# Performance work log

Measured on AMD Instinct MI355X. Metric: run time of the kernel, lower is better.

## Reference

```python
import jax, jax.numpy as jnp
import numpy as np

B, E, S = 64, 256, 32        # batch, projection_size (=MHA embed dim), seq_l
H = 16                        # MHA heads
D_FINAL = 10                  # label space
K_CLASSES = D_FINAL * (D_FINAL - 1) // 2 + 1  # 46, header output dim
N_PATIENTS = 8
P_PAIRS = N_PATIENTS * (B // N_PATIENTS) ** 2  # 512 same-patient pairs (static)


def _pair_lookup(D):
    # class id of sorted label pair: (0,0)->0, then (a,b) a<b in lexicographic
    # order, matching torch.unique(rows of triu meshgrid) ordering.
    lut = np.zeros((D, D), np.int32)
    idx = 1
    for a in range(D):
        for b in range(a + 1, D):
            lut[a, b] = idx
            lut[b, a] = idx
            idx += 1
    return lut


def setup_inputs():
    ks = jax.random.split(jax.random.key(0), 10)
    s = 1.0 / np.sqrt(E)
    return {
        "features": jax.random.normal(ks[0], (B, E, S), jnp.float32),
        "labels0": jax.random.randint(ks[1], (B,), 0, D_FINAL, jnp.int32),
        "labels1": (jnp.arange(B, dtype=jnp.int32) // (B // N_PATIENTS)),
        "in_proj_w": jax.random.normal(ks[2], (3 * E, E), jnp.float32) * s,
        "in_proj_b": jax.random.normal(ks[3], (3 * E,), jnp.float32) * 0.01,
        "out_proj_w": jax.random.normal(ks[4], (E, E), jnp.float32) * s,
        "out_proj_b": jax.random.normal(ks[5], (E,), jnp.float32) * 0.01,
        "final_w": jax.random.normal(ks[6], (1, S), jnp.float32) * (1.0 / np.sqrt(S)),
        "final_b": jax.random.normal(ks[7], (1,), jnp.float32) * 0.01,
        "header_w": jax.random.normal(ks[8], (K_CLASSES, E), jnp.float32) * s,
        "header_b": jax.random.normal(ks[9], (K_CLASSES,), jnp.float32) * 0.01,
    }


def reference(features, labels0, labels1, in_proj_w, in_proj_b, out_proj_w,
              out_proj_b, final_w, final_b, header_w, header_b):
    # ---- pair selection: (i, j) with same patient id (labels1) ----
    mask = (labels1[:, None] == labels1[None, :]).reshape(-1)  # (B*B,)
    sel = jnp.nonzero(mask, size=P_PAIRS, fill_value=0)[0]      # row-major order
    valid = (jnp.arange(P_PAIRS) < mask.sum()).astype(jnp.float32)
    i_idx, j_idx = sel // B, sel % B                            # (P,), (P,)

    # ---- pair class labels: sorted (l_i, l_j), equal labels -> (0, 0) ----
    a, b = labels0[i_idx], labels0[j_idx]
    eq = a == b
    lo = jnp.where(eq, 0, jnp.minimum(a, b))
    hi = jnp.where(eq, 0, jnp.maximum(a, b))
    lut = jnp.asarray(_pair_lookup(D_FINAL))
    y = lut[lo, hi]                                             # (P,) class ids

    # ---- gather pair features; torch permutes to (2, P, seq_l, C) ----
    q_in = jnp.transpose(features[i_idx], (0, 2, 1))  # (P, S, E) query
    kv_in = jnp.transpose(features[j_idx], (0, 2, 1))  # (P, S, E) key/value

    # ---- MultiheadAttention (eval, dropout off); L = pair axis P, N = S ----
    Wq, Wk, Wv = jnp.split(in_proj_w, 3, axis=0)
    bq, bk, bv = jnp.split(in_proj_b, 3, axis=0)
    hd = E // H
    q = (q_in @ Wq.T + bq).reshape(P_PAIRS, S, H, hd)
    k = (kv_in @ Wk.T + bk).reshape(P_PAIRS, S, H, hd)
    v = (kv_in @ Wv.T + bv).reshape(P_PAIRS, S, H, hd)
    scores = jnp.einsum('lshd,mshd->shlm', q, k) / np.sqrt(hd)  # (S,H,P,P)
    attn = jax.nn.softmax(scores, axis=-1)
    o = jnp.einsum('shlm,mshd->lshd', attn, v).reshape(P_PAIRS, S, E)
    o = o @ out_proj_w.T + out_proj_b                           # (P, S, E)

    # ---- backbone.final: Linear over the seq axis (S -> 1), squeeze ----
    h = jnp.einsum('pse,s->pe', o, final_w[0]) + final_b[0]     # (P, E)
    logits = h @ header_w.T + header_b                          # (P, K)

    # ---- inverse-frequency class weights over selected pairs ----
    counts = jnp.zeros(K_CLASSES, jnp.float32).at[y].add(valid)
    w = jnp.where(counts > 0, 1.0 / jnp.maximum(counts, 1.0), 0.0)

    # ---- weighted cross-entropy (torch semantics: / sum of weights) ----
    nll = -jax.nn.log_softmax(logits, axis=-1)[jnp.arange(P_PAIRS), y]
    wy = w[y] * valid
    loss = jnp.sum(wy * nll) / jnp.sum(wy)
    return loss
```

## Files before the change

### kernel.cpp

```cpp
#include <hip/hip_runtime.h>
#include <math.h>

#define B_ 64
#define E_ 256
#define S_ 32
#define H_ 16
#define P_ 512
#define KC_ 46

#define WS_CM     0
#define WS_WK     256
#define WS_INVDEN 3328
#define WS_C      3392
#define WS_M      3584
#define WS_WB     16384
#define WS_XF     114688
#define WS_OPART  1949696

typedef short bf16x8 __attribute__((ext_vector_type(8)));
typedef float f32x4  __attribute__((ext_vector_type(4)));

__device__ __forceinline__ ushort f2bf(float f) {
  unsigned u = __float_as_uint(f);
  u = (u + 0x7FFFu + ((u >> 16) & 1u)) >> 16;
  return (ushort)u;
}

__global__ __launch_bounds__(256) void k_prep(
    const float* __restrict__ feat, const float* __restrict__ w,
    const int* __restrict__ labels0, const int* __restrict__ labels1,
    const float* __restrict__ wout, const float* __restrict__ bout,
    const float* __restrict__ fw, const float* __restrict__ fbi,
    const float* __restrict__ hw, const float* __restrict__ hb,
    float* __restrict__ ws, float* __restrict__ out) {
  __shared__ float sm[8448];
  const int bid = blockIdx.x, t = threadIdx.x;
  if (bid < 24) {
    const float4* src = (const float4*)w;
    ushort* dstW = (ushort*)(ws + WS_WB);
#pragma unroll
    for (int i = 0; i < 8; ++i) {
      int idx = bid*2048 + i*256 + t;
      float4 v = src[idx];
      ushort4 o;
      o.x = f2bf(v.x); o.y = f2bf(v.y); o.z = f2bf(v.z); o.w = f2bf(v.w);
      *(ushort4*)(dstW + (size_t)idx*4) = o;
    }
  } else if (bid < 88) {
    const int b = bid - 24;
    const float4* fb = (const float4*)(feat + (size_t)b*(E_*S_));
#pragma unroll
    for (int i = 0; i < 8; ++i) {
      int idx = i*256 + t; int e = idx >> 3, s4 = (idx & 7)*4;
      float4 v = fb[idx];
      sm[e*33 + s4+0] = v.x; sm[e*33 + s4+1] = v.y;
      sm[e*33 + s4+2] = v.z; sm[e*33 + s4+3] = v.w;
    }
    __syncthreads();
    const int s = t >> 3, eb = (t & 7) * 32;
    ushort* dstX = (ushort*)(ws + WS_XF) + (size_t)s*(B_*E_) + (size_t)b*E_ + eb;
#pragma unroll
    for (int g = 0; g < 4; ++g) {
      ushort tmp[8];
#pragma unroll
      for (int u = 0; u < 8; ++u) tmp[u] = f2bf(sm[(eb + g*8 + u)*33 + s]);
      *(uint4*)(dstX + g*8) = *(uint4*)tmp;
    }
  } else if (bid == 88) {
    float* csh = sm;
    float* cls = sm + 64;
    float* wsh = sm + 112;
    float* den = sm + 160;
    float* Wk  = sm + 192;
    int* scan = (int*)(sm + 3200);
    int* l0   = (int*)(sm + 3456);
    int* l1   = (int*)(sm + 3520);
    int* seli = (int*)(sm + 3584);
    int* selj = (int*)(sm + 4096);
    if (t < 64) { l0[t] = labels0[t]; l1[t] = labels1[t]; csh[t] = 0.f; }
    if (t < KC_) cls[t] = 0.f;
    if (t == 0) den[0] = 0.f;
    for (int i = t; i < 2944; i += 256) Wk[i] = 0.f;
    __syncthreads();
    unsigned bits = 0; int c = 0;
    for (int u = 0; u < 16; ++u) {
      int idx = t*16 + u;
      if (l1[idx>>6] == l1[idx&63]) { bits |= 1u<<u; ++c; }
    }
    scan[t] = c; __syncthreads();
    for (int off = 1; off < 256; off <<= 1) {
      int v = (t >= off) ? scan[t-off] : 0;
      __syncthreads();
      scan[t] += v;
      __syncthreads();
    }
    const int total = scan[255];
    int rank = scan[t] - c;
    for (int p = t; p < P_; p += 256)
      if (p >= total) { seli[p] = 0; selj[p] = 0; }
    for (int u = 0; u < 16; ++u) {
      if (bits & (1u<<u)) {
        if (rank < P_) { int idx = t*16+u; seli[rank] = idx>>6; selj[rank] = idx&63; }
        ++rank;
      }
    }
    __syncthreads();
    int ii[2], yy[2]; float vv[2];
#pragma unroll
    for (int r = 0; r < 2; ++r) {
      int p = t + r*256;
      int i = seli[p], j = selj[p];
      atomicAdd(&csh[j], 1.0f);
      int la = l0[i], lb = l0[j];
      int y;
      if (la == lb) y = 0;
      else {
        int lo = la < lb ? la : lb, hi = la < lb ? lb : la;
        y = 1 + lo*9 - (lo*(lo-1))/2 + (hi-lo-1);
      }
      float v = (p < total) ? 1.f : 0.f;
      if (v > 0.f) atomicAdd(&cls[y], 1.f);
      ii[r] = i; yy[r] = y; vv[r] = v;
    }
    __syncthreads();
    if (t < KC_) {
      float cv = cls[t];
      wsh[t] = cv > 0.f ? 1.0f/cv : 0.f;
      if (cv > 0.f) atomicAdd(den, 1.0f);
    }
    __syncthreads();
#pragma unroll
    for (int r = 0; r < 2; ++r)
      if (vv[r] > 0.f) atomicAdd(&Wk[ii[r]*KC_ + yy[r]], wsh[yy[r]]);
    __syncthreads();
    if (t < 64) ws[WS_CM + t] = csh[t];
    for (int i = t; i < 2944; i += 256) ws[WS_WK + i] = Wk[i];
    if (t == 0) ws[WS_INVDEN] = 1.0f / den[0];
  } else if (bid < 135) {
    int k = bid - 89;
    float* hwsh = sm;
    float* redA = sm + 256;
    float* redB = sm + 512;
    hwsh[t] = hw[k*E_ + t];
    __syncthreads();
    float a0 = 0.f;
#pragma unroll 8
    for (int e = 0; e < E_; ++e) a0 = fmaf(hwsh[e], wout[e*E_ + t], a0);
    ws[WS_M + k*E_ + t] = a0;
    redA[t] = hwsh[t];
    redB[t] = hwsh[t]*bout[t];
    __syncthreads();
    for (int off = 128; off > 0; off >>= 1) {
      if (t < off) { redA[t] += redA[t+off]; redB[t] += redB[t+off]; }
      __syncthreads();
    }
    if (t == 0) {
      float sfw = 0.f;
      for (int s = 0; s < S_; ++s) sfw += fw[s];
      ws[WS_C + k] = fbi[0]*redA[0] + sfw*redB[0] + hb[k];
    }
  } else {
    if (t == 0) out[0] = 0.f;
  }
}

__global__ __launch_bounds__(256) void k_attn(
    const float* __restrict__ bias, const float* __restrict__ fw,
    float* __restrict__ ws) {
  __shared__ float qT[16*68], kT[16*68], vs[64*20], sc[64*68], cm[64];
  const int s = blockIdx.x >> 4, h = blockIdx.x & 15;
  const int t = threadIdx.x;
  const int w = t >> 6, L = t & 63, lane16 = L & 15, quad = L >> 4;
  const int a = t >> 2, dq = t & 3;
  {
    const short* WB = (const short*)(ws + WS_WB);
    const short* XF = (const short*)(ws + WS_XF);
    const short* brow  = XF + (size_t)s*(B_*E_) + (size_t)(w*16 + lane16)*E_ + quad*8;
    const short* arowQ = WB + (size_t)(      h*16 + lane16)*E_ + quad*8;
    const short* arowK = WB + (size_t)(256 + h*16 + lane16)*E_ + quad*8;
    const short* arowV = WB + (size_t)(512 + h*16 + lane16)*E_ + quad*8;
    f32x4 accQ = {0.f,0.f,0.f,0.f}, accK = {0.f,0.f,0.f,0.f}, accV = {0.f,0.f,0.f,0.f};
#pragma unroll
    for (int k = 0; k < 8; ++k) {
      bf16x8 bv = *(const bf16x8*)(brow  + k*32);
      bf16x8 aq = *(const bf16x8*)(arowQ + k*32);
      bf16x8 ak = *(const bf16x8*)(arowK + k*32);
      bf16x8 av = *(const bf16x8*)(arowV + k*32);
      accQ = __builtin_amdgcn_mfma_f32_16x16x32_bf16(aq, bv, accQ, 0, 0, 0);
      accK = __builtin_amdgcn_mfma_f32_16x16x32_bf16(ak, bv, accK, 0, 0, 0);
      accV = __builtin_amdgcn_mfma_f32_16x16x32_bf16(av, bv, accV, 0, 0, 0);
    }
    float4 bq = *(const float4*)(bias +        h*16 + quad*4);
    float4 bk = *(const float4*)(bias + 256 + h*16 + quad*4);
    float4 bv2 = *(const float4*)(bias + 512 + h*16 + quad*4);
    const float bqa[4] = {bq.x,bq.y,bq.z,bq.w};
    const float bka[4] = {bk.x,bk.y,bk.z,bk.w};
    const float bva[4] = {bv2.x,bv2.y,bv2.z,bv2.w};
    const int ag = w*16 + lane16;
#pragma unroll
    for (int r = 0; r < 4; ++r) {
      int d = quad*4 + r;
      qT[d*68 + ag] = (accQ[r] + bqa[r]) * 0.25f;
      kT[d*68 + ag] =  accK[r] + bka[r];
      vs[ag*20 + d] =  accV[r] + bva[r];
    }
  }
  if (t < 64) cm[t] = ws[WS_CM + t];
  __syncthreads();
  {
    const int ta = t & 15, tb = t >> 4;
    float sa[4][4];
#pragma unroll
    for (int r = 0; r < 4; ++r)
#pragma unroll
      for (int c = 0; c < 4; ++c) sa[r][c] = 0.f;
#pragma unroll
    for (int d = 0; d < 16; ++d) {
      float4 qv = *(float4*)(qT + d*68 + ta*4);
      float4 kv = *(float4*)(kT + d*68 + tb*4);
      float qr[4] = {qv.x,qv.y,qv.z,qv.w};
      float kc[4] = {kv.x,kv.y,kv.z,kv.w};
#pragma unroll
      for (int r = 0; r < 4; ++r)
#pragma unroll
        for (int c = 0; c < 4; ++c) sa[r][c] = fmaf(qr[r], kc[c], sa[r][c]);
    }
#pragma unroll
    for (int r = 0; r < 4; ++r)
      *(float4*)(sc + (ta*4+r)*68 + tb*4) =
          make_float4(sa[r][0], sa[r][1], sa[r][2], sa[r][3]);
  }
  __syncthreads();
  {
    float pv[16], cmv[16];
#pragma unroll
    for (int i4 = 0; i4 < 4; ++i4) {
      float4 v = *(float4*)(sc + a*68 + dq*16 + i4*4);
      pv[i4*4+0] = v.x; pv[i4*4+1] = v.y; pv[i4*4+2] = v.z; pv[i4*4+3] = v.w;
    }
#pragma unroll
    for (int i = 0; i < 16; ++i) cmv[i] = cm[dq*16 + i];
    float Mx = -1e30f;
#pragma unroll
    for (int i = 0; i < 16; ++i) if (cmv[i] > 0.f) Mx = fmaxf(Mx, pv[i]);
    Mx = fmaxf(Mx, __shfl_xor(Mx, 1));
    Mx = fmaxf(Mx, __shfl_xor(Mx, 2));
    float z = 0.f;
#pragma unroll
    for (int i = 0; i < 16; ++i) {
      float e = (cmv[i] > 0.f) ? cmv[i]*__expf(pv[i]-Mx) : 0.f;
      pv[i] = e; z += e;
    }
    z += __shfl_xor(z, 1);
    z += __shfl_xor(z, 2);
    float rz = 1.0f / z;
#pragma unroll
    for (int i4 = 0; i4 < 4; ++i4)
      *(float4*)(sc + a*68 + dq*16 + i4*4) =
          make_float4(pv[i4*4+0]*rz, pv[i4*4+1]*rz,
                      pv[i4*4+2]*rz, pv[i4*4+3]*rz);
  }
  __syncthreads();
  {
    const int g = t >> 6, l = t & 63;
    const int ar = g*16 + (l >> 2), d4 = (l & 3)*4;
    float o0 = 0.f, o1 = 0.f, o2 = 0.f, o3 = 0.f;
#pragma unroll 4
    for (int b4 = 0; b4 < 64; b4 += 4) {
      float4 p4 = *(float4*)(sc + ar*68 + b4);
      float4 va = *(float4*)(vs + (b4+0)*20 + d4);
      float4 vb = *(float4*)(vs + (b4+1)*20 + d4);
      float4 vc = *(float4*)(vs + (b4+2)*20 + d4);
      float4 vd = *(float4*)(vs + (b4+3)*20 + d4);
      o0 = fmaf(p4.x, va.x, fmaf(p4.y, vb.x, fmaf(p4.z, vc.x, fmaf(p4.w, vd.x, o0))));
      o1 = fmaf(p4.x, va.y, fmaf(p4.y, vb.y, fmaf(p4.z, vc.y, fmaf(p4.w, vd.y, o1))));
      o2 = fmaf(p4.x, va.z, fmaf(p4.y, vb.z, fmaf(p4.z, vc.z, fmaf(p4.w, vd.z, o2))));
      o3 = fmaf(p4.x, va.w, fmaf(p4.y, vb.w, fmaf(p4.z, vc.w, fmaf(p4.w, vd.w, o3))));
    }
    const float fwS = fw[s];
    float* dst = ws + WS_OPART + (size_t)s*(H_*B_*16) + h*(B_*16) + t*4;
    *(float4*)dst = make_float4(fwS*o0, fwS*o1, fwS*o2, fwS*o3);
  }
}

__global__ __launch_bounds__(256) void k_final(
    const float* __restrict__ ws, float* __restrict__ out) {
  const int aa = blockIdx.x, t = threadIdx.x;
  __shared__ float oh[256], lg[64];
  {
    const float* op = ws + WS_OPART + (t>>4)*(B_*16) + aa*16 + (t&15);
    float acc = 0.f;
#pragma unroll
    for (int s = 0; s < S_; ++s) acc += op[(size_t)s*(H_*B_*16)];
    oh[t] = acc;
  }
  __syncthreads();
  const int k = t >> 2, q = t & 3;
  if (k < KC_) {
    float lv = 0.f;
    const float4* M4 = (const float4*)(ws + WS_M + k*E_ + q*64);
    const float4* o4 = (const float4*)(oh + q*64);
#pragma unroll
    for (int j = 0; j < 16; ++j) {
      float4 m = M4[j], o = o4[j];
      lv = fmaf(m.x, o.x, lv); lv = fmaf(m.y, o.y, lv);
      lv = fmaf(m.z, o.z, lv); lv = fmaf(m.w, o.w, lv);
    }
    lv += __shfl_xor(lv, 1);
    lv += __shfl_xor(lv, 2);
    if (q == 0) lg[k] = lv + ws[WS_C + k];
  }
  __syncthreads();
  if (t < 64) {
    float x = (t < KC_) ? lg[t] : -1e30f;
    float Mx = x;
#pragma unroll
    for (int off = 1; off < 64; off <<= 1) Mx = fmaxf(Mx, __shfl_xor(Mx, off));
    float z = (t < KC_) ? __expf(x - Mx) : 0.f;
#pragma unroll
    for (int off = 1; off < 64; off <<= 1) z += __shfl_xor(z, off);
    float lse = Mx + __logf(z);
    float term = (t < KC_) ? ws[WS_WK + aa*KC_ + t] * (lse - x) : 0.f;
#pragma unroll
    for (int off = 1; off < 64; off <<= 1) term += __shfl_xor(term, off);
    if (t == 0) atomicAdd(out, term * ws[WS_INVDEN]);
  }
}

extern "C" void kernel_launch(void* const* d_in, const int* in_sizes, int n_in,
                              void* d_out, int out_size, void* d_ws, size_t ws_size,
                              hipStream_t stream) {
  const float* feat    = (const float*)d_in[0];
  const int*   labels0 = (const int*)d_in[1];
  const int*   labels1 = (const int*)d_in[2];
  const float* ipw     = (const float*)d_in[3];
  const float* ipb     = (const float*)d_in[4];
  const float* opw     = (const float*)d_in[5];
  const float* opb     = (const float*)d_in[6];
  const float* fw      = (const float*)d_in[7];
  const float* fbi     = (const float*)d_in[8];
  const float* hw      = (const float*)d_in[9];
  const float* hb      = (const float*)d_in[10];
  float* out = (float*)d_out;
  float* ws  = (float*)d_ws;

  k_prep<<<136, 256, 0, stream>>>(feat, ipw, labels0, labels1, opw, opb, fw,
                                  fbi, hw, hb, ws, out);
  k_attn<<<512, 256, 0, stream>>>(ipb, fw, ws);
  k_final<<<64, 256, 0, stream>>>(ws, out);
}
```

Measured before the change: 105.4 us.

## Move pair-selection and output-projection work from prep into attention and final kernels

```diff
diff --git a/kernel.cpp b/kernel.cpp
--- a/kernel.cpp
+++ b/kernel.cpp
@@ -8,11 +8,6 @@
 #define P_ 512
 #define KC_ 46
 
-#define WS_CM     0
-#define WS_WK     256
-#define WS_INVDEN 3328
-#define WS_C      3392
-#define WS_M      3584
 #define WS_WB     16384
 #define WS_XF     114688
 #define WS_OPART  1949696
@@ -26,12 +21,14 @@
   return (ushort)u;
 }
 
+__device__ __forceinline__ int pairclass(int la, int lb) {
+  if (la == lb) return 0;
+  int lo = la < lb ? la : lb, hi = la < lb ? lb : la;
+  return 1 + lo*9 - (lo*(lo-1))/2 + (hi - lo - 1);
+}
+
 __global__ __launch_bounds__(256) void k_prep(
     const float* __restrict__ feat, const float* __restrict__ w,
-    const int* __restrict__ labels0, const int* __restrict__ labels1,
-    const float* __restrict__ wout, const float* __restrict__ bout,
-    const float* __restrict__ fw, const float* __restrict__ fbi,
-    const float* __restrict__ hw, const float* __restrict__ hb,
     float* __restrict__ ws, float* __restrict__ out) {
   __shared__ float sm[8448];
   const int bid = blockIdx.x, t = threadIdx.x;
@@ -66,99 +63,6 @@
       for (int u = 0; u < 8; ++u) tmp[u] = f2bf(sm[(eb + g*8 + u)*33 + s]);
       *(uint4*)(dstX + g*8) = *(uint4*)tmp;
     }
-  } else if (bid == 88) {
-    float* csh = sm;
-    float* cls = sm + 64;
-    float* wsh = sm + 112;
-    float* den = sm + 160;
-    float* Wk  = sm + 192;
-    int* scan = (int*)(sm + 3200);
-    int* l0   = (int*)(sm + 3456);
-    int* l1   = (int*)(sm + 3520);
-    int* seli = (int*)(sm + 3584);
-    int* selj = (int*)(sm + 4096);
-    if (t < 64) { l0[t] = labels0[t]; l1[t] = labels1[t]; csh[t] = 0.f; }
-    if (t < KC_) cls[t] = 0.f;
-    if (t == 0) den[0] = 0.f;
-    for (int i = t; i < 2944; i += 256) Wk[i] = 0.f;
-    __syncthreads();
-    unsigned bits = 0; int c = 0;
-    for (int u = 0; u < 16; ++u) {
-      int idx = t*16 + u;
-      if (l1[idx>>6] == l1[idx&63]) { bits |= 1u<<u; ++c; }
-    }
-    scan[t] = c; __syncthreads();
-    for (int off = 1; off < 256; off <<= 1) {
-      int v = (t >= off) ? scan[t-off] : 0;
-      __syncthreads();
-      scan[t] += v;
-      __syncthreads();
-    }
-    const int total = scan[255];
-    int rank = scan[t] - c;
-    for (int p = t; p < P_; p += 256)
-      if (p >= total) { seli[p] = 0; selj[p] = 0; }
-    for (int u = 0; u < 16; ++u) {
-      if (bits & (1u<<u)) {
-        if (rank < P_) { int idx = t*16+u; seli[rank] = idx>>6; selj[rank] = idx&63; }
-        ++rank;
-      }
-    }
-    __syncthreads();
-    int ii[2], yy[2]; float vv[2];
-#pragma unroll
-    for (int r = 0; r < 2; ++r) {
-      int p = t + r*256;
-      int i = seli[p], j = selj[p];
-      atomicAdd(&csh[j], 1.0f);
-      int la = l0[i], lb = l0[j];
-      int y;
-      if (la == lb) y = 0;
-      else {
-        int lo = la < lb ? la : lb, hi = la < lb ? lb : la;
-        y = 1 + lo*9 - (lo*(lo-1))/2 + (hi-lo-1);
-      }
-      float v = (p < total) ? 1.f : 0.f;
-      if (v > 0.f) atomicAdd(&cls[y], 1.f);
-      ii[r] = i; yy[r] = y; vv[r] = v;
-    }
-    __syncthreads();
-    if (t < KC_) {
-      float cv = cls[t];
-      wsh[t] = cv > 0.f ? 1.0f/cv : 0.f;
-      if (cv > 0.f) atomicAdd(den, 1.0f);
-    }
-    __syncthreads();
-#pragma unroll
-    for (int r = 0; r < 2; ++r)
-      if (vv[r] > 0.f) atomicAdd(&Wk[ii[r]*KC_ + yy[r]], wsh[yy[r]]);
-    __syncthreads();
-    if (t < 64) ws[WS_CM + t] = csh[t];
-    for (int i = t; i < 2944; i += 256) ws[WS_WK + i] = Wk[i];
-    if (t == 0) ws[WS_INVDEN] = 1.0f / den[0];
-  } else if (bid < 135) {
-    int k = bid - 89;
-    float* hwsh = sm;
-    float* redA = sm + 256;
-    float* redB = sm + 512;
-    hwsh[t] = hw[k*E_ + t];
-    __syncthreads();
-    float a0 = 0.f;
-#pragma unroll 8
-    for (int e = 0; e < E_; ++e) a0 = fmaf(hwsh[e], wout[e*E_ + t], a0);
-    ws[WS_M + k*E_ + t] = a0;
-    redA[t] = hwsh[t];
-    redB[t] = hwsh[t]*bout[t];
-    __syncthreads();
-    for (int off = 128; off > 0; off >>= 1) {
-      if (t < off) { redA[t] += redA[t+off]; redB[t] += redB[t+off]; }
-      __syncthreads();
-    }
-    if (t == 0) {
-      float sfw = 0.f;
-      for (int s = 0; s < S_; ++s) sfw += fw[s];
-      ws[WS_C + k] = fbi[0]*redA[0] + sfw*redB[0] + hb[k];
-    }
   } else {
     if (t == 0) out[0] = 0.f;
   }
@@ -166,12 +70,14 @@
 
 __global__ __launch_bounds__(256) void k_attn(
     const float* __restrict__ bias, const float* __restrict__ fw,
-    float* __restrict__ ws) {
+    const int* __restrict__ labels1, float* __restrict__ ws) {
   __shared__ float qT[16*68], kT[16*68], vs[64*20], sc[64*68], cm[64];
+  __shared__ int l1s[64], gsA[64], rjA[64], rsA[64];
   const int s = blockIdx.x >> 4, h = blockIdx.x & 15;
   const int t = threadIdx.x;
   const int w = t >> 6, L = t & 63, lane16 = L & 15, quad = L >> 4;
   const int a = t >> 2, dq = t & 3;
+  int myl1 = (t < 64) ? labels1[t] : 0;
   {
     const short* WB = (const short*)(ws + WS_WB);
     const short* XF = (const short*)(ws + WS_XF);
@@ -190,8 +96,8 @@
       accK = __builtin_amdgcn_mfma_f32_16x16x32_bf16(ak, bv, accK, 0, 0, 0);
       accV = __builtin_amdgcn_mfma_f32_16x16x32_bf16(av, bv, accV, 0, 0, 0);
     }
-    float4 bq = *(const float4*)(bias +        h*16 + quad*4);
-    float4 bk = *(const float4*)(bias + 256 + h*16 + quad*4);
+    float4 bq  = *(const float4*)(bias +       h*16 + quad*4);
+    float4 bk  = *(const float4*)(bias + 256 + h*16 + quad*4);
     float4 bv2 = *(const float4*)(bias + 512 + h*16 + quad*4);
     const float bqa[4] = {bq.x,bq.y,bq.z,bq.w};
     const float bka[4] = {bk.x,bk.y,bk.z,bk.w};
@@ -205,7 +111,29 @@
       vs[ag*20 + d] =  accV[r] + bva[r];
     }
   }
-  if (t < 64) cm[t] = ws[WS_CM + t];
+  if (t < 64) {
+    l1s[t] = myl1;
+    int gj = l1s[t];
+    int gs_ = 0, rj_ = 0;
+#pragma unroll 8
+    for (int j2 = 0; j2 < 64; ++j2) {
+      int m = (l1s[j2] == gj) ? 1 : 0;
+      gs_ += m;
+      if (j2 < t) rj_ += m;
+    }
+    gsA[t] = gs_; rjA[t] = rj_;
+    int rs_ = 0;
+#pragma unroll 8
+    for (int i = 0; i < 64; ++i) if (i < t) rs_ += gsA[i];
+    rsA[t] = rs_;
+    int cnt = 0;
+#pragma unroll 8
+    for (int i = 0; i < 64; ++i)
+      if (l1s[i] == gj && rsA[i] + rj_ < P_) ++cnt;
+    int total = rsA[63] + gsA[63];
+    if (t == 0 && total < P_) cnt += P_ - total;
+    cm[t] = (float)cnt;
+  }
   __syncthreads();
   {
     const int ta = t & 15, tb = t >> 4;
@@ -284,31 +212,94 @@
 }
 
 __global__ __launch_bounds__(256) void k_final(
-    const float* __restrict__ ws, float* __restrict__ out) {
+    const float* __restrict__ ws, const int* __restrict__ labels0,
+    const int* __restrict__ labels1, const float* __restrict__ wout,
+    const float* __restrict__ bout, const float* __restrict__ fw,
+    const float* __restrict__ fbi, const float* __restrict__ hw,
+    const float* __restrict__ hb, float* __restrict__ out) {
   const int aa = blockIdx.x, t = threadIdx.x;
-  __shared__ float oh[256], lg[64];
+  __shared__ float ohs[256], hs[256], lg[64], fws[32];
+  __shared__ float cls[48], wsh[48], wk[48], denf;
+  __shared__ int l0s[64], l1s[64], gsA[64], rjA[64], rsA[64];
+  if (t < 64) { l0s[t] = labels0[t]; l1s[t] = labels1[t]; }
+  if (t < 32) fws[t] = fw[t];
+  if (t < 48) { cls[t] = 0.f; wk[t] = 0.f; }
+  if (t == 0) denf = 0.f;
+  __syncthreads();
+  if (t < 64) {
+    int gj = l1s[t];
+    int gs_ = 0, rj_ = 0;
+#pragma unroll 8
+    for (int j2 = 0; j2 < 64; ++j2) {
+      int m = (l1s[j2] == gj) ? 1 : 0;
+      gs_ += m;
+      if (j2 < t) rj_ += m;
+    }
+    gsA[t] = gs_; rjA[t] = rj_;
+    int rs_ = 0;
+#pragma unroll 8
+    for (int i = 0; i < 64; ++i) if (i < t) rs_ += gsA[i];
+    rsA[t] = rs_;
+  }
+  __syncthreads();
+  for (int u = 0; u < 16; ++u) {
+    int idx = t*16 + u; int i = idx >> 6, j = idx & 63;
+    if (l1s[i] == l1s[j] && rsA[i] + rjA[j] < P_)
+      atomicAdd(&cls[pairclass(l0s[i], l0s[j])], 1.f);
+  }
+  __syncthreads();
+  if (t < KC_) {
+    float cv = cls[t];
+    wsh[t] = cv > 0.f ? 1.0f/cv : 0.f;
+    if (cv > 0.f) atomicAdd(&denf, 1.0f);
+  }
+  __syncthreads();
+  if (t < 64) {
+    if (l1s[t] == l1s[aa] && rsA[aa] + rjA[t] < P_) {
+      int y = pairclass(l0s[aa], l0s[t]);
+      atomicAdd(&wk[y], wsh[y]);
+    }
+  }
   {
     const float* op = ws + WS_OPART + (t>>4)*(B_*16) + aa*16 + (t&15);
     float acc = 0.f;
 #pragma unroll
     for (int s = 0; s < S_; ++s) acc += op[(size_t)s*(H_*B_*16)];
-    oh[t] = acc;
-  }
-  __syncthreads();
-  const int k = t >> 2, q = t & 3;
-  if (k < KC_) {
-    float lv = 0.f;
-    const float4* M4 = (const float4*)(ws + WS_M + k*E_ + q*64);
-    const float4* o4 = (const float4*)(oh + q*64);
-#pragma unroll
-    for (int j = 0; j < 16; ++j) {
-      float4 m = M4[j], o = o4[j];
-      lv = fmaf(m.x, o.x, lv); lv = fmaf(m.y, o.y, lv);
-      lv = fmaf(m.z, o.z, lv); lv = fmaf(m.w, o.w, lv);
-    }
-    lv += __shfl_xor(lv, 1);
-    lv += __shfl_xor(lv, 2);
-    if (q == 0) lg[k] = lv + ws[WS_C + k];
+    ohs[t] = acc;
+  }
+  __syncthreads();
+  {
+    float sfw = 0.f;
+#pragma unroll
+    for (int s2 = 0; s2 < S_; ++s2) sfw += fws[s2];
+    float gacc = 0.f;
+    const float4* wr = (const float4*)(wout + (size_t)t*E_);
+    const float4* o4 = (const float4*)ohs;
+#pragma unroll 8
+    for (int j = 0; j < 64; ++j) {
+      float4 wv = wr[j], ov = o4[j];
+      gacc = fmaf(wv.x, ov.x, gacc); gacc = fmaf(wv.y, ov.y, gacc);
+      gacc = fmaf(wv.z, ov.z, gacc); gacc = fmaf(wv.w, ov.w, gacc);
+    }
+    hs[t] = gacc + bout[t]*sfw + fbi[0];
+  }
+  __syncthreads();
+  {
+    const int k = t >> 2, q = t & 3;
+    if (k < KC_) {
+      float lv = 0.f;
+      const float4* h4 = (const float4*)(hw + (size_t)k*E_ + q*64);
+      const float4* s4 = (const float4*)(hs + q*64);
+#pragma unroll
+      for (int j = 0; j < 16; ++j) {
+        float4 m = h4[j], o = s4[j];
+        lv = fmaf(m.x, o.x, lv); lv = fmaf(m.y, o.y, lv);
+        lv = fmaf(m.z, o.z, lv); lv = fmaf(m.w, o.w, lv);
+      }
+      lv += __shfl_xor(lv, 1);
+      lv += __shfl_xor(lv, 2);
+      if (q == 0) lg[k] = lv + hb[k];
+    }
   }
   __syncthreads();
   if (t < 64) {
@@ -320,10 +311,10 @@
 #pragma unroll
     for (int off = 1; off < 64; off <<= 1) z += __shfl_xor(z, off);
     float lse = Mx + __logf(z);
-    float term = (t < KC_) ? ws[WS_WK + aa*KC_ + t] * (lse - x) : 0.f;
+    float term = (t < KC_) ? wk[t] * (lse - x) : 0.f;
 #pragma unroll
     for (int off = 1; off < 64; off <<= 1) term += __shfl_xor(term, off);
-    if (t == 0) atomicAdd(out, term * ws[WS_INVDEN]);
+    if (t == 0) atomicAdd(out, term / denf);
   }
 }
 
@@ -344,8 +335,8 @@
   float* out = (float*)d_out;
   float* ws  = (float*)d_ws;
 
-  k_prep<<<136, 256, 0, stream>>>(feat, ipw, labels0, labels1, opw, opb, fw,
-                                  fbi, hw, hb, ws, out);
-  k_attn<<<512, 256, 0, stream>>>(ipb, fw, ws);
-  k_final<<<64, 256, 0, stream>>>(ws, out);
-}
+  k_prep<<<89, 256, 0, stream>>>(feat, ipw, ws, out);
+  k_attn<<<512, 256, 0, stream>>>(ipb, fw, labels1, ws);
+  k_final<<<64, 256, 0, stream>>>(ws, labels0, labels1, opw, opb, fw, fbi,
+                                  hw, hb, out);
+}
```

Result: slower. 109.3 us (+3.8%).
